# Performance work log

Measured on AMD Instinct MI355X. Metric: run time of the kernel, lower is better.

## Reference

```python
import jax, jax.numpy as jnp
import numpy as np


def setup_inputs() -> dict:
    key = jax.random.key(0)
    kq, kk, kv = jax.random.split(key, 3)
    shape = (2, 8, 1024, 64)  # [B, H, L, D]
    return {
        "q": jax.random.normal(kq, shape, dtype=jnp.float32),
        "k": jax.random.normal(kk, shape, dtype=jnp.float32),
        "v": jax.random.normal(kv, shape, dtype=jnp.float32),
    }


def reference(q, k, v):
    B, H, L, D = q.shape
    eps = 1e-6
    q = jax.nn.relu(q).reshape(B * H, L, D)
    k = jax.nn.relu(k).reshape(B * H, L, D)
    v = jax.nn.relu(v).reshape(B * H, L, D)

    # cosFormer positional reweighting: pi/2 * (i+1)/L
    idx = (jnp.pi / 2) * jnp.arange(1, L + 1, dtype=q.dtype) / L  # [L]
    s = jnp.sin(idx)[None, :, None]  # [1, L, 1]
    c = jnp.cos(idx)[None, :, None]

    q_ = jnp.concatenate([q * s, q * c], axis=-1)  # [N, L, 2D]
    k_ = jnp.concatenate([k * s, k * c], axis=-1)  # [N, L, 2D]

    # causal linear attention via cumulative kv outer product
    kv = jnp.einsum("nld,nlm->nldm", k_, v)        # [N, L, 2D, D]
    kv_cum = jnp.cumsum(kv, axis=1)                  # [N, L, 2D, D]
    qkv = jnp.einsum("nld,nldm->nlm", q_, kv_cum)  # [N, L, D]

    k_cum = jnp.cumsum(k_, axis=1)                   # [N, L, 2D]
    denom = jnp.clip(jnp.einsum("nld,nld->nl", q_, k_cum), eps, None)

    out = qkv / denom[..., None]
    return out.reshape(B, H, L, D)
```

## Files before the change

kernel.cpp:

```cpp
#include <hip/hip_runtime.h>
#include <hip/hip_fp16.h>

#define N_HEADS 16
#define L_SEQ   1024
#define D_HEAD  64
#define D2      128
#define T_CHUNK 32
#define N_CHUNK (L_SEQ / T_CHUNK)
#define KV_ELEMS (D2 * D_HEAD)
#define PK_UINTS (KV_ELEMS / 2)

#define PQ 132
#define PS 136
#define PV 36

#define SINCOS_SCALE 1.53398078788564122971e-3f

typedef _Float16 f16_t;
typedef __attribute__((ext_vector_type(4))) _Float16 f16x4;
typedef __attribute__((ext_vector_type(4))) float f32x4;

__device__ __forceinline__ f32x4 mfma16(f16x4 a, f16x4 b, f32x4 c) {
    return __builtin_amdgcn_mfma_f32_16x16x16f16(a, b, c, 0, 0, 0);
}

__device__ __forceinline__ unsigned int packh2(float a, float b) {
    __half2 h = __floats2half2_rn(a, b);
    return __builtin_bit_cast(unsigned int, h);
}
__device__ __forceinline__ float2 unpackh2(unsigned int u) {
    __half2 h = __builtin_bit_cast(__half2, u);
    return __half22float2(h);
}

__device__ __forceinline__ float red8_dpp(float x) {
    x += __int_as_float(__builtin_amdgcn_mov_dpp(__float_as_int(x), 0xB1, 0xF, 0xF, true));
    x += __int_as_float(__builtin_amdgcn_mov_dpp(__float_as_int(x), 0x4E, 0xF, 0xF, true));
    x += __int_as_float(__builtin_amdgcn_mov_dpp(__float_as_int(x), 0x141, 0xF, 0xF, true));
    return x;
}
__device__ __forceinline__ float red16_dpp(float x) {
    x += __int_as_float(__builtin_amdgcn_mov_dpp(__float_as_int(x), 0xB1, 0xF, 0xF, true));
    x += __int_as_float(__builtin_amdgcn_mov_dpp(__float_as_int(x), 0x4E, 0xF, 0xF, true));
    x += __int_as_float(__builtin_amdgcn_mov_dpp(__float_as_int(x), 0x141, 0xF, 0xF, true));
    x += __int_as_float(__builtin_amdgcn_mov_dpp(__float_as_int(x), 0x140, 0xF, 0xF, true));
    return x;
}

__global__ __launch_bounds__(256, 2) void k1_chunk_sums(
    const float* __restrict__ k, const float* __restrict__ v,
    unsigned int* __restrict__ sumkv, float* __restrict__ sumk)
{
    __shared__ __attribute__((aligned(16))) f16_t k16t[D2][PV];
    __shared__ __attribute__((aligned(16))) f16_t vt1[D_HEAD][PV];
    __shared__ __attribute__((aligned(16))) f16_t ob[D_HEAD][PS];
    __shared__ float s_tab[T_CHUNK], c_tab[T_CHUNK];

    const int c = blockIdx.x, n = blockIdx.y;
    const int tid = threadIdx.x;
    const int base = (n * L_SEQ + c * T_CHUNK) * D_HEAD;

    if (tid < T_CHUNK) {
        float th = SINCOS_SCALE * (float)(c * T_CHUNK + tid + 1);
        s_tab[tid] = __sinf(th);
        c_tab[tid] = __cosf(th);
    }
    __syncthreads();

    const float4* k4g = (const float4*)(k + base);
    const float4* v4g = (const float4*)(v + base);
#pragma unroll
    for (int j = 0; j < 2; ++j) {
        int i4 = j * 256 + tid;
        int l = i4 >> 4, d = (i4 & 15) << 2;
        float4 kk = k4g[i4], vv = v4g[i4];
        kk.x = fmaxf(kk.x, 0.f); kk.y = fmaxf(kk.y, 0.f);
        kk.z = fmaxf(kk.z, 0.f); kk.w = fmaxf(kk.w, 0.f);
        vv.x = fmaxf(vv.x, 0.f); vv.y = fmaxf(vv.y, 0.f);
        vv.z = fmaxf(vv.z, 0.f); vv.w = fmaxf(vv.w, 0.f);
        float s = s_tab[l], cs = c_tab[l];
        k16t[d+0][l]    = (f16_t)(kk.x*s);  k16t[d+1][l]    = (f16_t)(kk.y*s);
        k16t[d+2][l]    = (f16_t)(kk.z*s);  k16t[d+3][l]    = (f16_t)(kk.w*s);
        k16t[d+64][l]   = (f16_t)(kk.x*cs); k16t[d+65][l]   = (f16_t)(kk.y*cs);
        k16t[d+66][l]   = (f16_t)(kk.z*cs); k16t[d+67][l]   = (f16_t)(kk.w*cs);
        vt1[d+0][l] = (f16_t)vv.x; vt1[d+1][l] = (f16_t)vv.y;
        vt1[d+2][l] = (f16_t)vv.z; vt1[d+3][l] = (f16_t)vv.w;
    }
    __syncthreads();

    if (tid < D2) {
        const f16x4* row = (const f16x4*)&k16t[tid][0];
        float acc = 0.f;
#pragma unroll
        for (int i = 0; i < 8; ++i) {
            f16x4 x = row[i];
            acc += ((float)x[0] + (float)x[1]) + ((float)x[2] + (float)x[3]);
        }
        sumk[(n * N_CHUNK + c) * D2 + tid] = acc;
    }

    const int wave = tid >> 6, lane = tid & 63;
    const int fr = lane & 15;
    const int fk = (lane >> 4) << 2;

    f16x4 a0 = *(const f16x4*)&vt1[wave * 16 + fr][fk];
    f16x4 a1 = *(const f16x4*)&vt1[wave * 16 + fr][16 + fk];

    f32x4 acc[8];
#pragma unroll
    for (int nt = 0; nt < 8; ++nt) acc[nt] = (f32x4){0.f, 0.f, 0.f, 0.f};
#pragma unroll
    for (int nt = 0; nt < 8; ++nt) {
        f16x4 b0 = *(const f16x4*)&k16t[nt * 16 + fr][fk];
        f16x4 b1 = *(const f16x4*)&k16t[nt * 16 + fr][16 + fk];
        acc[nt] = mfma16(a0, b0, acc[nt]);
        acc[nt] = mfma16(a1, b1, acc[nt]);
    }

#pragma unroll
    for (int nt = 0; nt < 8; ++nt)
#pragma unroll
        for (int r = 0; r < 4; ++r)
            ob[wave * 16 + fk + r][nt * 16 + fr] = (f16_t)acc[nt][r];
    __syncthreads();

    uint4* dst = (uint4*)(sumkv + (size_t)(n * N_CHUNK + c) * PK_UINTS);
#pragma unroll
    for (int t = 0; t < 4; ++t) {
        int u = t * 256 + tid;
        dst[u] = *(const uint4*)&ob[u >> 4][(u & 15) * 8];
    }
}

__global__ __launch_bounds__(256) void k2_prefix(
    unsigned int* __restrict__ sumkv, float* __restrict__ sumk)
{
    const int x = blockIdx.x, n = blockIdx.y;
    const int tid = threadIdx.x;

    if (x < 8) {
        uint2* base = (uint2*)(sumkv + (size_t)n * N_CHUNK * PK_UINTS) + x * 256 + tid;
        uint2 t[N_CHUNK];
#pragma unroll
        for (int c = 0; c < N_CHUNK; ++c) t[c] = base[c * (PK_UINTS / 2)];
        float r0 = 0.f, r1 = 0.f, r2 = 0.f, r3 = 0.f;
#pragma unroll
        for (int c = 0; c < N_CHUNK; ++c) {
            uint2 cur = t[c];
            base[c * (PK_UINTS / 2)] = make_uint2(packh2(r0, r1), packh2(r2, r3));
            float2 lo = unpackh2(cur.x), hi = unpackh2(cur.y);
            r0 += lo.x; r1 += lo.y; r2 += hi.x; r3 += hi.y;
        }
    } else if (tid < D2) {
        float* bk = sumk + n * N_CHUNK * D2 + tid;
        float t[N_CHUNK];
#pragma unroll
        for (int c = 0; c < N_CHUNK; ++c) t[c] = bk[c * D2];
        float r = 0.f;
#pragma unroll
        for (int c = 0; c < N_CHUNK; ++c) { bk[c * D2] = r; r += t[c]; }
    }
}

__global__ __launch_bounds__(256, 2) void k3_output(
    const float* __restrict__ q, const float* __restrict__ k,
    const float* __restrict__ v, const unsigned int* __restrict__ sumkv,
    const float* __restrict__ sumk, float* __restrict__ out)
{
    __shared__ __attribute__((aligned(16))) f16_t q16[T_CHUNK][PQ];
    __shared__ __attribute__((aligned(16))) f16_t k16[T_CHUNK][PQ];
    __shared__ __attribute__((aligned(16))) f16_t vt[D_HEAD][PV];
    __shared__ __attribute__((aligned(16))) f16_t s0t[D_HEAD][PS];
    __shared__ __attribute__((aligned(16))) f16_t pmat[T_CHUNK][PV];
    __shared__ float kc0[D2];
    __shared__ float den0_s[T_CHUNK], dpA[T_CHUNK], dpB[T_CHUNK], rden[T_CHUNK];
    __shared__ float s_tab[T_CHUNK], c_tab[T_CHUNK];

    const int c = blockIdx.x, n = blockIdx.y;
    const int tid = threadIdx.x;
    const int base = (n * L_SEQ + c * T_CHUNK) * D_HEAD;

    if (tid < T_CHUNK) {
        float th = SINCOS_SCALE * (float)(c * T_CHUNK + tid + 1);
        s_tab[tid] = __sinf(th);
        c_tab[tid] = __cosf(th);
    }
    __syncthreads();

    const float4* q4g = (const float4*)(q + base);
    const float4* k4g = (const float4*)(k + base);
    const float4* v4g = (const float4*)(v + base);
#pragma unroll
    for (int j = 0; j < 2; ++j) {
        int i4 = j * 256 + tid;
        int l = i4 >> 4, d = (i4 & 15) << 2;
        float4 kk = k4g[i4], qq = q4g[i4], vv = v4g[i4];
        kk.x = fmaxf(kk.x, 0.f); kk.y = fmaxf(kk.y, 0.f);
        kk.z = fmaxf(kk.z, 0.f); kk.w = fmaxf(kk.w, 0.f);
        qq.x = fmaxf(qq.x, 0.f); qq.y = fmaxf(qq.y, 0.f);
        qq.z = fmaxf(qq.z, 0.f); qq.w = fmaxf(qq.w, 0.f);
        vv.x = fmaxf(vv.x, 0.f); vv.y = fmaxf(vv.y, 0.f);
        vv.z = fmaxf(vv.z, 0.f); vv.w = fmaxf(vv.w, 0.f);
        float s = s_tab[l], cs = c_tab[l];
        q16[l][d+0]    = (f16_t)(qq.x*s);  q16[l][d+1]    = (f16_t)(qq.y*s);
        q16[l][d+2]    = (f16_t)(qq.z*s);  q16[l][d+3]    = (f16_t)(qq.w*s);
        q16[l][d+64]   = (f16_t)(qq.x*cs); q16[l][d+65]   = (f16_t)(qq.y*cs);
        q16[l][d+66]   = (f16_t)(qq.z*cs); q16[l][d+67]   = (f16_t)(qq.w*cs);
        k16[l][d+0]    = (f16_t)(kk.x*s);  k16[l][d+1]    = (f16_t)(kk.y*s);
        k16[l][d+2]    = (f16_t)(kk.z*s);  k16[l][d+3]    = (f16_t)(kk.w*s);
        k16[l][d+64]   = (f16_t)(kk.x*cs); k16[l][d+65]   = (f16_t)(kk.y*cs);
        k16[l][d+66]   = (f16_t)(kk.z*cs); k16[l][d+67]   = (f16_t)(kk.w*cs);
        vt[d+0][l] = (f16_t)vv.x; vt[d+1][l] = (f16_t)vv.y;
        vt[d+2][l] = (f16_t)vv.z; vt[d+3][l] = (f16_t)vv.w;
    }
    {
        const uint4* pkv = (const uint4*)(sumkv + (size_t)(n * N_CHUNK + c) * PK_UINTS);
#pragma unroll
        for (int jj = 0; jj < 4; ++jj) {
            int u = jj * 256 + tid;
            int pos = u << 3;
            *(uint4*)&s0t[pos >> 7][pos & 127] = pkv[u];
        }
    }
    if (tid < D2) kc0[tid] = sumk[(n * N_CHUNK + c) * D2 + tid];
    __syncthreads();

    {
        int l = tid >> 3, seg = (tid & 7) << 4;
        float a = 0.f;
#pragma unroll
        for (int i = 0; i < 16; ++i) a += (float)q16[l][seg + i] * kc0[seg + i];
        a = red8_dpp(a);
        if ((tid & 7) == 0) den0_s[l] = a;
    }

    const int wave = tid >> 6, lane = tid & 63;
    const int fr = lane & 15;
    const int fk = (lane >> 4) << 2;
    const int rowq = (lane >> 4) << 2;

    if (wave < 3) {
        const int mt = (wave == 0) ? 0 : 1;
        const int nt = (wave == 2) ? 1 : 0;
        f32x4 sa = {0.f, 0.f, 0.f, 0.f};
#pragma unroll
        for (int ks = 0; ks < 8; ++ks) {
            f16x4 a = *(const f16x4*)&q16[mt * 16 + fr][ks * 16 + fk];
            f16x4 b = *(const f16x4*)&k16[nt * 16 + fr][ks * 16 + fk];
            sa = mfma16(a, b, sa);
        }
#pragma unroll
        for (int r = 0; r < 4; ++r) {
            int row = rowq + r;
            float mv = (mt > nt || fr <= row) ? sa[r] : 0.f;
            pmat[mt * 16 + row][nt * 16 + fr] = (f16_t)mv;
            float rs = red16_dpp(mv);
            if (fr == 0) {
                if (wave == 2) dpB[16 + row] = rs;
                else dpA[mt * 16 + row] = rs;
            }
        }
    } else {
        int row = lane >> 2, colb = 16 + ((lane & 3) << 2);
        *(uint2*)&pmat[row][colb] = make_uint2(0u, 0u);
    }
    __syncthreads();

    if (tid < T_CHUNK) {
        float den = den0_s[tid] + dpA[tid] + ((tid >= 16) ? dpB[tid] : 0.f);
        rden[tid] = 1.f / fmaxf(den, 1e-6f);
    }

    const int mt = wave >> 1;
    const int nt0 = (wave & 1) << 1, nt1 = nt0 + 1;
    f32x4 o0 = {0.f, 0.f, 0.f, 0.f}, o1 = {0.f, 0.f, 0.f, 0.f};
#pragma unroll
    for (int ks = 0; ks < 8; ++ks) {
        f16x4 a  = *(const f16x4*)&q16[mt * 16 + fr][ks * 16 + fk];
        f16x4 b0 = *(const f16x4*)&s0t[nt0 * 16 + fr][ks * 16 + fk];
        f16x4 b1 = *(const f16x4*)&s0t[nt1 * 16 + fr][ks * 16 + fk];
        o0 = mfma16(a, b0, o0);
        o1 = mfma16(a, b1, o1);
    }
#pragma unroll
    for (int ks = 0; ks < 2; ++ks) {
        f16x4 a  = *(const f16x4*)&pmat[mt * 16 + fr][ks * 16 + fk];
        f16x4 b0 = *(const f16x4*)&vt[nt0 * 16 + fr][ks * 16 + fk];
        f16x4 b1 = *(const f16x4*)&vt[nt1 * 16 + fr][ks * 16 + fk];
        o0 = mfma16(a, b0, o0);
        o1 = mfma16(a, b1, o1);
    }
    __syncthreads();

    float* og = out + base;
#pragma unroll
    for (int r = 0; r < 4; ++r) {
        int row = mt * 16 + rowq + r;
        float rd = rden[row];
        og[row * D_HEAD + nt0 * 16 + fr] = o0[r] * rd;
        og[row * D_HEAD + nt1 * 16 + fr] = o1[r] * rd;
    }
}

extern "C" void kernel_launch(void* const* d_in, const int* in_sizes, int n_in,
                              void* d_out, int out_size, void* d_ws, size_t ws_size,
                              hipStream_t stream) {
    (void)in_sizes; (void)n_in; (void)out_size; (void)ws_size;
    const float* q = (const float*)d_in[0];
    const float* k = (const float*)d_in[1];
    const float* v = (const float*)d_in[2];
    float* out = (float*)d_out;

    unsigned int* sumkv = (unsigned int*)d_ws;
    float* sumk = (float*)(sumkv + (size_t)N_HEADS * N_CHUNK * PK_UINTS);

    dim3 grid(N_CHUNK, N_HEADS);
    k1_chunk_sums<<<grid, 256, 0, stream>>>(k, v, sumkv, sumk);
    dim3 grid2(9, N_HEADS);
    k2_prefix<<<grid2, 256, 0, stream>>>(sumkv, sumk);
    k3_output<<<grid, 256, 0, stream>>>(q, k, v, sumkv, sumk, out);
}
```

Baseline: 75.59 us.

## Double chunk length and pass preprocessed fp16 k/v from chunk-sum kernel to output kernel

The sequence chunk grows from 32 to 64 rows, and both the chunk-sum and output kernels move to 512-thread blocks, with MFMA work reassigned across eight waves. The chunk-sum kernel now writes the relu'd, sin/cos-weighted fp16 k features and the transposed fp16 v to workspace. The output kernel reads those instead of reloading and reprocessing fp32 k and v. The aim is to halve the number of chunks and prefix steps and to drop repeated preprocessing, at the cost of extra workspace writes and fewer, larger blocks.

```diff
diff --git a/kernel.cpp b/kernel.cpp
--- a/kernel.cpp
+++ b/kernel.cpp
@@ -5,14 +5,14 @@
 #define L_SEQ   1024
 #define D_HEAD  64
 #define D2      128
-#define T_CHUNK 32
+#define T_CHUNK 64
 #define N_CHUNK (L_SEQ / T_CHUNK)
 #define KV_ELEMS (D2 * D_HEAD)
 #define PK_UINTS (KV_ELEMS / 2)
 
-#define PQ 132
-#define PS 136
-#define PV 36
+#define P136 136
+#define P76  76
+#define P68  68
 
 #define SINCOS_SCALE 1.53398078788564122971e-3f
 
@@ -47,13 +47,15 @@
     return x;
 }
 
-__global__ __launch_bounds__(256, 2) void k1_chunk_sums(
+__global__ __launch_bounds__(512, 2) void k1_chunk_sums(
     const float* __restrict__ k, const float* __restrict__ v,
-    unsigned int* __restrict__ sumkv, float* __restrict__ sumk)
+    unsigned int* __restrict__ sumkv, unsigned int* __restrict__ kx,
+    unsigned int* __restrict__ vx, float* __restrict__ sumk)
 {
-    __shared__ __attribute__((aligned(16))) f16_t k16t[D2][PV];
-    __shared__ __attribute__((aligned(16))) f16_t vt1[D_HEAD][PV];
-    __shared__ __attribute__((aligned(16))) f16_t ob[D_HEAD][PS];
+    __shared__ __attribute__((aligned(16))) f16_t k16t[D2][P68];
+    __shared__ __attribute__((aligned(16))) f16_t vt1[D_HEAD][P76];
+    __shared__ __attribute__((aligned(16))) f16_t k16row[T_CHUNK][P136];
+    __shared__ __attribute__((aligned(16))) f16_t ob[D_HEAD][P136];
     __shared__ float s_tab[T_CHUNK], c_tab[T_CHUNK];
 
     const int c = blockIdx.x, n = blockIdx.y;
@@ -71,7 +73,7 @@
     const float4* v4g = (const float4*)(v + base);
 #pragma unroll
     for (int j = 0; j < 2; ++j) {
-        int i4 = j * 256 + tid;
+        int i4 = j * 512 + tid;
         int l = i4 >> 4, d = (i4 & 15) << 2;
         float4 kk = k4g[i4], vv = v4g[i4];
         kk.x = fmaxf(kk.x, 0.f); kk.y = fmaxf(kk.y, 0.f);
@@ -79,10 +81,16 @@
         vv.x = fmaxf(vv.x, 0.f); vv.y = fmaxf(vv.y, 0.f);
         vv.z = fmaxf(vv.z, 0.f); vv.w = fmaxf(vv.w, 0.f);
         float s = s_tab[l], cs = c_tab[l];
-        k16t[d+0][l]    = (f16_t)(kk.x*s);  k16t[d+1][l]    = (f16_t)(kk.y*s);
-        k16t[d+2][l]    = (f16_t)(kk.z*s);  k16t[d+3][l]    = (f16_t)(kk.w*s);
-        k16t[d+64][l]   = (f16_t)(kk.x*cs); k16t[d+65][l]   = (f16_t)(kk.y*cs);
-        k16t[d+66][l]   = (f16_t)(kk.z*cs); k16t[d+67][l]   = (f16_t)(kk.w*cs);
+        f16_t a0 = (f16_t)(kk.x*s),  a1 = (f16_t)(kk.y*s),
+              a2 = (f16_t)(kk.z*s),  a3 = (f16_t)(kk.w*s);
+        f16_t b0 = (f16_t)(kk.x*cs), b1 = (f16_t)(kk.y*cs),
+              b2 = (f16_t)(kk.z*cs), b3 = (f16_t)(kk.w*cs);
+        k16t[d+0][l] = a0;  k16t[d+1][l] = a1;  k16t[d+2][l] = a2;  k16t[d+3][l] = a3;
+        k16t[d+64][l] = b0; k16t[d+65][l] = b1; k16t[d+66][l] = b2; k16t[d+67][l] = b3;
+        f16x4 ra; ra[0]=a0; ra[1]=a1; ra[2]=a2; ra[3]=a3;
+        f16x4 rb; rb[0]=b0; rb[1]=b1; rb[2]=b2; rb[3]=b3;
+        *(f16x4*)&k16row[l][d]      = ra;
+        *(f16x4*)&k16row[l][d + 64] = rb;
         vt1[d+0][l] = (f16_t)vv.x; vt1[d+1][l] = (f16_t)vv.y;
         vt1[d+2][l] = (f16_t)vv.z; vt1[d+3][l] = (f16_t)vv.w;
     }
@@ -92,42 +100,55 @@
         const f16x4* row = (const f16x4*)&k16t[tid][0];
         float acc = 0.f;
 #pragma unroll
-        for (int i = 0; i < 8; ++i) {
+        for (int i = 0; i < 16; ++i) {
             f16x4 x = row[i];
             acc += ((float)x[0] + (float)x[1]) + ((float)x[2] + (float)x[3]);
         }
         sumk[(n * N_CHUNK + c) * D2 + tid] = acc;
     }
 
+    {
+        uint4* kxd = (uint4*)kx + (size_t)(n * L_SEQ + c * T_CHUNK) * 16;
+#pragma unroll
+        for (int t = 0; t < 2; ++t) {
+            int u = t * 512 + tid;
+            kxd[u] = *(const uint4*)&k16row[u >> 4][(u & 15) * 8];
+        }
+        uint2* vxd = (uint2*)vx + (size_t)(n * N_CHUNK + c) * 1024;
+#pragma unroll
+        for (int t = 0; t < 2; ++t) {
+            int u = t * 512 + tid;
+            vxd[u] = *(const uint2*)&vt1[u >> 4][(u & 15) * 4];
+        }
+    }
+
     const int wave = tid >> 6, lane = tid & 63;
-    const int fr = lane & 15;
-    const int fk = (lane >> 4) << 2;
-
-    f16x4 a0 = *(const f16x4*)&vt1[wave * 16 + fr][fk];
-    f16x4 a1 = *(const f16x4*)&vt1[wave * 16 + fr][16 + fk];
-
-    f32x4 acc[8];
-#pragma unroll
-    for (int nt = 0; nt < 8; ++nt) acc[nt] = (f32x4){0.f, 0.f, 0.f, 0.f};
-#pragma unroll
-    for (int nt = 0; nt < 8; ++nt) {
-        f16x4 b0 = *(const f16x4*)&k16t[nt * 16 + fr][fk];
-        f16x4 b1 = *(const f16x4*)&k16t[nt * 16 + fr][16 + fk];
-        acc[nt] = mfma16(a0, b0, acc[nt]);
-        acc[nt] = mfma16(a1, b1, acc[nt]);
-    }
-
-#pragma unroll
-    for (int nt = 0; nt < 8; ++nt)
+    const int fr = lane & 15, fk = (lane >> 4) << 2;
+    const int mt = wave >> 1, ntg = (wave & 1) * 4;
+
+    f32x4 acc[4];
+#pragma unroll
+    for (int t = 0; t < 4; ++t) acc[t] = (f32x4){0.f, 0.f, 0.f, 0.f};
+#pragma unroll
+    for (int ks = 0; ks < 4; ++ks) {
+        f16x4 a = *(const f16x4*)&vt1[mt * 16 + fr][ks * 16 + fk];
+#pragma unroll
+        for (int t = 0; t < 4; ++t) {
+            f16x4 b = *(const f16x4*)&k16t[(ntg + t) * 16 + fr][ks * 16 + fk];
+            acc[t] = mfma16(a, b, acc[t]);
+        }
+    }
+#pragma unroll
+    for (int t = 0; t < 4; ++t)
 #pragma unroll
         for (int r = 0; r < 4; ++r)
-            ob[wave * 16 + fk + r][nt * 16 + fr] = (f16_t)acc[nt][r];
-    __syncthreads();
-
-    uint4* dst = (uint4*)(sumkv + (size_t)(n * N_CHUNK + c) * PK_UINTS);
-#pragma unroll
-    for (int t = 0; t < 4; ++t) {
-        int u = t * 256 + tid;
+            ob[mt * 16 + fk + r][(ntg + t) * 16 + fr] = (f16_t)acc[t][r];
+    __syncthreads();
+
+    uint4* dst = (uint4*)sumkv + (size_t)(n * N_CHUNK + c) * 1024;
+#pragma unroll
+    for (int t = 0; t < 2; ++t) {
+        int u = t * 512 + tid;
         dst[u] = *(const uint4*)&ob[u >> 4][(u & 15) * 8];
     }
 }
@@ -162,18 +183,18 @@
     }
 }
 
-__global__ __launch_bounds__(256, 2) void k3_output(
-    const float* __restrict__ q, const float* __restrict__ k,
-    const float* __restrict__ v, const unsigned int* __restrict__ sumkv,
+__global__ __launch_bounds__(512, 2) void k3_output(
+    const float* __restrict__ q, const unsigned int* __restrict__ kx,
+    const unsigned int* __restrict__ vx, const unsigned int* __restrict__ sumkv,
     const float* __restrict__ sumk, float* __restrict__ out)
 {
-    __shared__ __attribute__((aligned(16))) f16_t q16[T_CHUNK][PQ];
-    __shared__ __attribute__((aligned(16))) f16_t k16[T_CHUNK][PQ];
-    __shared__ __attribute__((aligned(16))) f16_t vt[D_HEAD][PV];
-    __shared__ __attribute__((aligned(16))) f16_t s0t[D_HEAD][PS];
-    __shared__ __attribute__((aligned(16))) f16_t pmat[T_CHUNK][PV];
+    __shared__ __attribute__((aligned(16))) f16_t q16[T_CHUNK][P136];
+    __shared__ __attribute__((aligned(16))) f16_t k16[T_CHUNK][P136];
+    __shared__ __attribute__((aligned(16))) f16_t vt[D_HEAD][P76];
+    __shared__ __attribute__((aligned(16))) f16_t s0t[D_HEAD][P136];
+    __shared__ __attribute__((aligned(16))) f16_t pmat[T_CHUNK][P76];
     __shared__ float kc0[D2];
-    __shared__ float den0_s[T_CHUNK], dpA[T_CHUNK], dpB[T_CHUNK], rden[T_CHUNK];
+    __shared__ float den0_s[T_CHUNK], dp[2][T_CHUNK], rden[T_CHUNK];
     __shared__ float s_tab[T_CHUNK], c_tab[T_CHUNK];
 
     const int c = blockIdx.x, n = blockIdx.y;
@@ -188,38 +209,37 @@
     __syncthreads();
 
     const float4* q4g = (const float4*)(q + base);
-    const float4* k4g = (const float4*)(k + base);
-    const float4* v4g = (const float4*)(v + base);
 #pragma unroll
     for (int j = 0; j < 2; ++j) {
-        int i4 = j * 256 + tid;
+        int i4 = j * 512 + tid;
         int l = i4 >> 4, d = (i4 & 15) << 2;
-        float4 kk = k4g[i4], qq = q4g[i4], vv = v4g[i4];
-        kk.x = fmaxf(kk.x, 0.f); kk.y = fmaxf(kk.y, 0.f);
-        kk.z = fmaxf(kk.z, 0.f); kk.w = fmaxf(kk.w, 0.f);
+        float4 qq = q4g[i4];
         qq.x = fmaxf(qq.x, 0.f); qq.y = fmaxf(qq.y, 0.f);
         qq.z = fmaxf(qq.z, 0.f); qq.w = fmaxf(qq.w, 0.f);
-        vv.x = fmaxf(vv.x, 0.f); vv.y = fmaxf(vv.y, 0.f);
-        vv.z = fmaxf(vv.z, 0.f); vv.w = fmaxf(vv.w, 0.f);
         float s = s_tab[l], cs = c_tab[l];
-        q16[l][d+0]    = (f16_t)(qq.x*s);  q16[l][d+1]    = (f16_t)(qq.y*s);
-        q16[l][d+2]    = (f16_t)(qq.z*s);  q16[l][d+3]    = (f16_t)(qq.w*s);
-        q16[l][d+64]   = (f16_t)(qq.x*cs); q16[l][d+65]   = (f16_t)(qq.y*cs);
-        q16[l][d+66]   = (f16_t)(qq.z*cs); q16[l][d+67]   = (f16_t)(qq.w*cs);
-        k16[l][d+0]    = (f16_t)(kk.x*s);  k16[l][d+1]    = (f16_t)(kk.y*s);
-        k16[l][d+2]    = (f16_t)(kk.z*s);  k16[l][d+3]    = (f16_t)(kk.w*s);
-        k16[l][d+64]   = (f16_t)(kk.x*cs); k16[l][d+65]   = (f16_t)(kk.y*cs);
-        k16[l][d+66]   = (f16_t)(kk.z*cs); k16[l][d+67]   = (f16_t)(kk.w*cs);
-        vt[d+0][l] = (f16_t)vv.x; vt[d+1][l] = (f16_t)vv.y;
-        vt[d+2][l] = (f16_t)vv.z; vt[d+3][l] = (f16_t)vv.w;
+        q16[l][d+0]  = (f16_t)(qq.x*s);  q16[l][d+1]  = (f16_t)(qq.y*s);
+        q16[l][d+2]  = (f16_t)(qq.z*s);  q16[l][d+3]  = (f16_t)(qq.w*s);
+        q16[l][d+64] = (f16_t)(qq.x*cs); q16[l][d+65] = (f16_t)(qq.y*cs);
+        q16[l][d+66] = (f16_t)(qq.z*cs); q16[l][d+67] = (f16_t)(qq.w*cs);
     }
     {
-        const uint4* pkv = (const uint4*)(sumkv + (size_t)(n * N_CHUNK + c) * PK_UINTS);
-#pragma unroll
-        for (int jj = 0; jj < 4; ++jj) {
-            int u = jj * 256 + tid;
-            int pos = u << 3;
-            *(uint4*)&s0t[pos >> 7][pos & 127] = pkv[u];
+        const uint4* kxs = (const uint4*)kx + (size_t)(n * L_SEQ + c * T_CHUNK) * 16;
+#pragma unroll
+        for (int t = 0; t < 2; ++t) {
+            int u = t * 512 + tid;
+            *(uint4*)&k16[u >> 4][(u & 15) * 8] = kxs[u];
+        }
+        const uint2* vxs = (const uint2*)vx + (size_t)(n * N_CHUNK + c) * 1024;
+#pragma unroll
+        for (int t = 0; t < 2; ++t) {
+            int u = t * 512 + tid;
+            *(uint2*)&vt[u >> 4][(u & 15) * 4] = vxs[u];
+        }
+        const uint4* pkv = (const uint4*)sumkv + (size_t)(n * N_CHUNK + c) * 1024;
+#pragma unroll
+        for (int t = 0; t < 2; ++t) {
+            int u = t * 512 + tid;
+            *(uint4*)&s0t[u >> 4][(u & 15) * 8] = pkv[u];
         }
     }
     if (tid < D2) kc0[tid] = sumk[(n * N_CHUNK + c) * D2 + tid];
@@ -235,58 +255,59 @@
     }
 
     const int wave = tid >> 6, lane = tid & 63;
-    const int fr = lane & 15;
-    const int fk = (lane >> 4) << 2;
-    const int rowq = (lane >> 4) << 2;
-
-    if (wave < 3) {
-        const int mt = (wave == 0) ? 0 : 1;
-        const int nt = (wave == 2) ? 1 : 0;
-        f32x4 sa = {0.f, 0.f, 0.f, 0.f};
-#pragma unroll
-        for (int ks = 0; ks < 8; ++ks) {
-            f16x4 a = *(const f16x4*)&q16[mt * 16 + fr][ks * 16 + fk];
-            f16x4 b = *(const f16x4*)&k16[nt * 16 + fr][ks * 16 + fk];
-            sa = mfma16(a, b, sa);
-        }
-#pragma unroll
-        for (int r = 0; r < 4; ++r) {
-            int row = rowq + r;
-            float mv = (mt > nt || fr <= row) ? sa[r] : 0.f;
-            pmat[mt * 16 + row][nt * 16 + fr] = (f16_t)mv;
-            float rs = red16_dpp(mv);
-            if (fr == 0) {
-                if (wave == 2) dpB[16 + row] = rs;
-                else dpA[mt * 16 + row] = rs;
+    const int fr = lane & 15, fk = (lane >> 4) << 2, rowq = fk;
+    const int mt = wave >> 1;
+    const int nt0 = (wave & 1) << 1;
+
+    {
+        float rs[4] = {0.f, 0.f, 0.f, 0.f};
+#pragma unroll
+        for (int t = 0; t < 2; ++t) {
+            int nt = nt0 + t;
+            if (mt >= nt) {
+                f32x4 sa = {0.f, 0.f, 0.f, 0.f};
+#pragma unroll
+                for (int ks = 0; ks < 8; ++ks) {
+                    f16x4 a = *(const f16x4*)&q16[mt * 16 + fr][ks * 16 + fk];
+                    f16x4 b = *(const f16x4*)&k16[nt * 16 + fr][ks * 16 + fk];
+                    sa = mfma16(a, b, sa);
+                }
+#pragma unroll
+                for (int r = 0; r < 4; ++r) {
+                    int row = rowq + r;
+                    float mv = (mt > nt || fr <= row) ? sa[r] : 0.f;
+                    pmat[mt * 16 + row][nt * 16 + fr] = (f16_t)mv;
+                    rs[r] += red16_dpp(mv);
+                }
+            } else {
+#pragma unroll
+                for (int r = 0; r < 4; ++r)
+                    pmat[mt * 16 + rowq + r][nt * 16 + fr] = (f16_t)0.f;
             }
         }
-    } else {
-        int row = lane >> 2, colb = 16 + ((lane & 3) << 2);
-        *(uint2*)&pmat[row][colb] = make_uint2(0u, 0u);
-    }
-    __syncthreads();
-
-    if (tid < T_CHUNK) {
-        float den = den0_s[tid] + dpA[tid] + ((tid >= 16) ? dpB[tid] : 0.f);
-        rden[tid] = 1.f / fmaxf(den, 1e-6f);
-    }
-
-    const int mt = wave >> 1;
-    const int nt0 = (wave & 1) << 1, nt1 = nt0 + 1;
+        if (fr == 0)
+#pragma unroll
+            for (int r = 0; r < 4; ++r) dp[wave & 1][mt * 16 + rowq + r] = rs[r];
+    }
+    __syncthreads();
+
+    if (tid < T_CHUNK)
+        rden[tid] = 1.f / fmaxf(den0_s[tid] + dp[0][tid] + dp[1][tid], 1e-6f);
+
     f32x4 o0 = {0.f, 0.f, 0.f, 0.f}, o1 = {0.f, 0.f, 0.f, 0.f};
 #pragma unroll
     for (int ks = 0; ks < 8; ++ks) {
         f16x4 a  = *(const f16x4*)&q16[mt * 16 + fr][ks * 16 + fk];
-        f16x4 b0 = *(const f16x4*)&s0t[nt0 * 16 + fr][ks * 16 + fk];
-        f16x4 b1 = *(const f16x4*)&s0t[nt1 * 16 + fr][ks * 16 + fk];
+        f16x4 b0 = *(const f16x4*)&s0t[(nt0 + 0) * 16 + fr][ks * 16 + fk];
+        f16x4 b1 = *(const f16x4*)&s0t[(nt0 + 1) * 16 + fr][ks * 16 + fk];
         o0 = mfma16(a, b0, o0);
         o1 = mfma16(a, b1, o1);
     }
 #pragma unroll
-    for (int ks = 0; ks < 2; ++ks) {
+    for (int ks = 0; ks < 4; ++ks) {
         f16x4 a  = *(const f16x4*)&pmat[mt * 16 + fr][ks * 16 + fk];
-        f16x4 b0 = *(const f16x4*)&vt[nt0 * 16 + fr][ks * 16 + fk];
-        f16x4 b1 = *(const f16x4*)&vt[nt1 * 16 + fr][ks * 16 + fk];
+        f16x4 b0 = *(const f16x4*)&vt[(nt0 + 0) * 16 + fr][ks * 16 + fk];
+        f16x4 b1 = *(const f16x4*)&vt[(nt0 + 1) * 16 + fr][ks * 16 + fk];
         o0 = mfma16(a, b0, o0);
         o1 = mfma16(a, b1, o1);
     }
@@ -297,8 +318,8 @@
     for (int r = 0; r < 4; ++r) {
         int row = mt * 16 + rowq + r;
         float rd = rden[row];
-        og[row * D_HEAD + nt0 * 16 + fr] = o0[r] * rd;
-        og[row * D_HEAD + nt1 * 16 + fr] = o1[r] * rd;
+        og[row * D_HEAD + (nt0 + 0) * 16 + fr] = o0[r] * rd;
+        og[row * D_HEAD + (nt0 + 1) * 16 + fr] = o1[r] * rd;
     }
 }
 
@@ -312,11 +333,13 @@
     float* out = (float*)d_out;
 
     unsigned int* sumkv = (unsigned int*)d_ws;
-    float* sumk = (float*)(sumkv + (size_t)N_HEADS * N_CHUNK * PK_UINTS);
+    unsigned int* kx    = sumkv + (size_t)N_HEADS * N_CHUNK * PK_UINTS;
+    unsigned int* vx    = kx + (size_t)N_HEADS * L_SEQ * D2 / 2;
+    float*        sumk  = (float*)(vx + (size_t)N_HEADS * N_CHUNK * T_CHUNK * D_HEAD / 2);
 
     dim3 grid(N_CHUNK, N_HEADS);
-    k1_chunk_sums<<<grid, 256, 0, stream>>>(k, v, sumkv, sumk);
+    k1_chunk_sums<<<grid, 512, 0, stream>>>(k, v, sumkv, kx, vx, sumk);
     dim3 grid2(9, N_HEADS);
     k2_prefix<<<grid2, 256, 0, stream>>>(sumkv, sumk);
-    k3_output<<<grid, 256, 0, stream>>>(q, k, v, sumkv, sumk, out);
-}
+    k3_output<<<grid, 512, 0, stream>>>(q, kx, vx, sumkv, sumk, out);
+}
```

After: 77.84 us. 3.0% more time.
